# Optimization experiments

Hardware: AMD Instinct MI355X
Metric: run time of the kernel (lower is better)

Reference implementation:

```python
import jax, jax.numpy as jnp
import numpy as np

B, S, D, H = 2048, 200, 128, 4
H1, H2 = 64, 32
F = 4 * D
TIME_DECAY = 0.1


def setup_inputs() -> dict:
    key = jax.random.key(0)
    ks = jax.random.split(key, 10)
    query = jax.random.normal(ks[0], (B, D), dtype=jnp.float32)
    keys = jax.random.normal(ks[1], (B, S, D), dtype=jnp.float32)
    keys_mask = jax.random.randint(ks[2], (B, S), 0, 2).astype(bool)
    keys_mask = keys_mask.at[:, 0].set(True)  # avoid fully-masked rows
    sc = 0.02
    # per-head MLP params, stacked over heads
    W1 = sc * jax.random.normal(ks[3], (H, H1, F), dtype=jnp.float32)
    b1 = jnp.zeros((H, H1), dtype=jnp.float32)
    a1 = 0.25 * jnp.ones((H,), dtype=jnp.float32)  # PReLU (default single param)
    W2 = sc * jax.random.normal(ks[4], (H, H2, H1), dtype=jnp.float32)
    b2 = jnp.zeros((H, H2), dtype=jnp.float32)
    a2 = 0.25 * jnp.ones((H,), dtype=jnp.float32)
    W3 = sc * jax.random.normal(ks[5], (H, H2), dtype=jnp.float32)
    b3 = jnp.zeros((H,), dtype=jnp.float32)
    Wo = sc * jax.random.normal(ks[6], (D, D), dtype=jnp.float32)
    bo = jnp.zeros((D,), dtype=jnp.float32)
    return {"query": query, "keys": keys, "keys_mask": keys_mask,
            "W1": W1, "b1": b1, "a1": a1, "W2": W2, "b2": b2, "a2": a2,
            "W3": W3, "b3": b3, "Wo": Wo, "bo": bo}


def reference(query, keys, keys_mask, W1, b1, a1, W2, b2, a2, W3, b3, Wo, bo):
    b, s, d = keys.shape
    q = query[:, None, :]                                    # [B,1,D]
    x = jnp.concatenate(
        [keys, jnp.broadcast_to(q, (b, s, d)), keys * q, keys - q], axis=-1)  # [B,S,4D]
    pos = jnp.arange(s, dtype=keys.dtype)
    tw = jnp.exp(TIME_DECAY * (pos - s + 1))                 # [S]
    # all heads batched: [B,H,S,H1]
    h = jnp.einsum('bsf,hdf->bhsd', x, W1) + b1[None, :, None, :]
    h = jnp.where(h >= 0, h, a1[None, :, None, None] * h)    # PReLU
    h = jnp.einsum('bhsd,hed->bhse', h, W2) + b2[None, :, None, :]
    h = jnp.where(h >= 0, h, a2[None, :, None, None] * h)
    scores = jnp.einsum('bhse,he->bhs', h, W3) + b3[None, :, None]
    scores = scores * tw[None, None, :]
    scores = jnp.where(keys_mask[:, None, :], scores, -1e9)
    w = jax.nn.softmax(scores, axis=-1)                      # [B,H,S]
    out_h = jnp.einsum('bhs,bsd->bhd', w, keys)              # [B,H,D]
    combined = out_h.mean(axis=1)                            # [B,D]
    output = combined @ Wo.T + bo                            # [B,D]
    avg_weights = w.mean(axis=1)                             # [B,S]
    return output, avg_weights
```

## Files before the change

kernel.cpp:

```cpp
#include <hip/hip_runtime.h>
#include <hip/hip_bf16.h>
#include <stdint.h>

#define Bsz 2048
#define Ssz 200
#define Dsz 128

typedef __attribute__((ext_vector_type(8))) short short8;
typedef __attribute__((ext_vector_type(4))) short short4v;
typedef __attribute__((ext_vector_type(4))) float f32x4;
typedef unsigned short ushort_t;
typedef unsigned int uint_t;

#define KEYS_OFF   0
#define SCB_OFF    28672
#define C1S_OFF    30720
#define B2S_OFF    31744
#define W3S_OFF    32256
#define SMEM_A     32768

#if defined(__has_builtin)
#if __has_builtin(__builtin_amdgcn_mfma_f32_16x16x16bf16_1k)
#define HAVE_MFMA16 1
#endif
#endif

__device__ __forceinline__ f32x4 mfma16(short4v a, short4v b, f32x4 c) {
#ifdef HAVE_MFMA16
    return __builtin_amdgcn_mfma_f32_16x16x16bf16_1k(a, b, c, 0, 0, 0);
#else
    f32x4 d;
    asm volatile("v_mfma_f32_16x16x16_bf16 %0, %1, %2, %3"
                 : "=&v"(d) : "v"(a), "v"(b), "v"(c));
    return d;
#endif
}

__device__ __forceinline__ ushort_t cvtbf(float x) {
    __hip_bfloat16 h = __float2bfloat16(x);
    ushort_t u;
    __builtin_memcpy(&u, &h, 2);
    return u;
}
__device__ __forceinline__ float bflo(uint_t kv) {
    union { uint_t u; float f; } v; v.u = kv << 16; return v.f;
}
__device__ __forceinline__ float bfhi(uint_t kv) {
    union { uint_t u; float f; } v; v.u = kv & 0xFFFF0000u; return v.f;
}

__global__ void prep_kernel(const float* __restrict__ W1, const float* __restrict__ W2,
                            const float* __restrict__ Wo,
                            float* __restrict__ W1sum, float* __restrict__ W1c,
                            float* __restrict__ W1diffR, float* __restrict__ WoT,
                            ushort_t* __restrict__ W2bf) {
    int i = blockIdx.x * blockDim.x + threadIdx.x;
    if (i < 32768) {
        int n = i >> 7, j = i & 127;
        float a  = W1[n * 512 + j];
        float dd = W1[n * 512 + 384 + j];
        W1sum[i] = a + dd;
        W1c[i]   = W1[n * 512 + 256 + j];
        W1diffR[i] = W1[n * 512 + 128 + j] - dd;
    }
    if (i < 16384) {
        int j = i >> 7, d = i & 127;
        WoT[i] = Wo[d * 128 + j];
    }
    if (i < 8192) W2bf[i] = cvtbf(W2[i]);
}

__global__ void w1effc1_kernel(const float* __restrict__ query, const float* __restrict__ W1sum,
                               const float* __restrict__ W1c, const float* __restrict__ W1diffR,
                               const float* __restrict__ b1,
                               ushort_t* __restrict__ W1g2, float* __restrict__ c1out) {
    __shared__ float qs[128];
    int b = blockIdx.x, t = threadIdx.x;
    if (t < 128) qs[t] = query[b * 128 + t];
    __syncthreads();
    {
        float acc = b1[t];
        const float4* wr  = (const float4*)(W1diffR + t * 128);
        const float4* qv4 = (const float4*)qs;
        #pragma unroll 8
        for (int j4 = 0; j4 < 32; ++j4) {
            float4 wv = wr[j4];
            float4 qq = qv4[j4];
            acc += wv.x * qq.x + wv.y * qq.y + wv.z * qq.z + wv.w * qq.w;
        }
        c1out[b * 256 + t] = acc;
    }
    ushort_t* wout = W1g2 + ((size_t)b << 15);
    #pragma unroll 2
    for (int it = 0; it < 16; ++it) {
        int o  = t + 256 * it;
        int t4 = o >> 10, lk = (o >> 8) & 3, n = o & 255;
        int k0 = t4 * 32 + lk * 8;
        const float4* ps = (const float4*)(W1sum + n * 128 + k0);
        const float4* pc = (const float4*)(W1c + n * 128 + k0);
        const float4* pq = (const float4*)(qs + k0);
        float4 s0 = ps[0], s1 = ps[1];
        float4 c0 = pc[0], c1f = pc[1];
        float4 q0 = pq[0], q1 = pq[1];
        short8 ov;
        ov[0] = (short)cvtbf(s0.x + c0.x * q0.x);
        ov[1] = (short)cvtbf(s0.y + c0.y * q0.y);
        ov[2] = (short)cvtbf(s0.z + c0.z * q0.z);
        ov[3] = (short)cvtbf(s0.w + c0.w * q0.w);
        ov[4] = (short)cvtbf(s1.x + c1f.x * q1.x);
        ov[5] = (short)cvtbf(s1.y + c1f.y * q1.y);
        ov[6] = (short)cvtbf(s1.z + c1f.z * q1.z);
        ov[7] = (short)cvtbf(s1.w + c1f.w * q1.w);
        *(short8*)(wout + (size_t)o * 8) = ov;
    }
}

__global__ void c1_kernel(const float* __restrict__ query, const float* __restrict__ W1diffR,
                          const float* __restrict__ b1, float* __restrict__ c1out) {
    int b = blockIdx.x, n = threadIdx.x;
    float acc = b1[n];
    const float4* wr  = (const float4*)(W1diffR + n * 128);
    const float4* qv4 = (const float4*)(query + b * 128);
    #pragma unroll 8
    for (int j4 = 0; j4 < 32; ++j4) {
        float4 wv = wr[j4];
        float4 qq = qv4[j4];
        acc += wv.x * qq.x + wv.y * qq.y + wv.z * qq.z + wv.w * qq.w;
    }
    c1out[b * 256 + n] = acc;
}

__device__ __forceinline__ void stage_all(char* smem, const float* keys,
                                          const float* c1ws, const float* b2g,
                                          const float* w3g, int bb, int half, int tid) {
    const float* kb = keys + (size_t)bb * Ssz * Dsz;
    const int rbase = half * 112;
    #pragma unroll 2
    for (int it = 0; it < 14; ++it) {
        int id = tid + 256 * it;
        int row = id >> 5, c4 = id & 31;
        int grow = rbase + row;
        float4 kv = {0.f, 0.f, 0.f, 0.f};
        if (grow < Ssz) kv = *(const float4*)(kb + (size_t)grow * Dsz + c4 * 4);
        uint2 p;
        p.x = (uint_t)cvtbf(kv.x) | ((uint_t)cvtbf(kv.y) << 16);
        p.y = (uint_t)cvtbf(kv.z) | ((uint_t)cvtbf(kv.w) << 16);
        int off = KEYS_OFF + (((row << 8) + (c4 << 3)) ^ ((row & 7) << 4));
        *(uint2*)(smem + off) = p;
    }
    ((float*)(smem + C1S_OFF))[tid] = c1ws[bb * 256 + tid];
    if (tid < 128) ((float*)(smem + B2S_OFF))[tid] = b2g[tid];
    else if (tid < 256) ((float*)(smem + W3S_OFF))[tid - 128] = w3g[tid - 128];
}

__device__ __forceinline__ void scores_body(char* smem, const short8* bfr,
                                            const int* kmask,
                                            const float* a1, const float* a2,
                                            const float* b3, const ushort_t* W2bf,
                                            float* scores_ws,
                                            float* numws, float* mdws,
                                            int bb, int half, int w, int l, int l15, int lk) {
    const int rbase = half * 112;

    const float a1v = a1[w];
    const float a2v = a2[w];
    const float b3v = b3[w];
    short4v w2a[2][4];
    #pragma unroll
    for (int nt2 = 0; nt2 < 2; ++nt2)
        #pragma unroll
        for (int kt = 0; kt < 4; ++kt)
            w2a[nt2][kt] = *(const short4v*)(W2bf + w * 2048 + (nt2 * 16 + l15) * 64
                                             + kt * 16 + lk * 4);

    __syncthreads();

    const f32x4 fz = {0.f, 0.f, 0.f, 0.f};
    float* scb = (float*)(smem + SCB_OFF + w * 512);
    const float* c1s = (const float*)(smem + C1S_OFF);
    const float* b2s = (const float*)(smem + B2S_OFF);
    const float* w3s = (const float*)(smem + W3S_OFF);
    const int ntiles = 7 - half;

    #pragma unroll 1
    for (int mi = 0; mi < ntiles; ++mi) {
        f32x4 acc[4];
        #pragma unroll
        for (int kt = 0; kt < 4; ++kt) acc[kt] = fz;
        #pragma unroll
        for (int t = 0; t < 4; ++t) {
            int lrow = mi * 16 + l15;
            int off = KEYS_OFF + (((lrow << 8) + (t * 64 + lk * 16)) ^ ((lrow & 7) << 4));
            short8 kfr = *(const short8*)(smem + off);
            #pragma unroll
            for (int kt = 0; kt < 4; ++kt)
                acc[kt] = __builtin_amdgcn_mfma_f32_16x16x32_bf16(bfr[t * 4 + kt], kfr, acc[kt], 0, 0, 0);
        }
        short4v pa[4];
        #pragma unroll
        for (int kt = 0; kt < 4; ++kt) {
            f32x4 c1q = *(const f32x4*)(c1s + w * 64 + kt * 16 + lk * 4);
            #pragma unroll
            for (int r = 0; r < 4; ++r) {
                float v = acc[kt][r] + c1q[r];
                v = (v >= 0.f) ? v : a1v * v;
                pa[kt][r] = (short)cvtbf(v);
            }
        }
        f32x4 acc2[2];
        acc2[0] = fz; acc2[1] = fz;
        #pragma unroll
        for (int kt = 0; kt < 4; ++kt) {
            acc2[0] = mfma16(w2a[0][kt], pa[kt], acc2[0]);
            acc2[1] = mfma16(w2a[1][kt], pa[kt], acc2[1]);
        }
        float sum = 0.f;
        #pragma unroll
        for (int nt2 = 0; nt2 < 2; ++nt2) {
            f32x4 b2q = *(const f32x4*)(b2s + w * 32 + nt2 * 16 + lk * 4);
            f32x4 w3q = *(const f32x4*)(w3s + w * 32 + nt2 * 16 + lk * 4);
            #pragma unroll
            for (int r = 0; r < 4; ++r) {
                float v = acc2[nt2][r] + b2q[r];
                v = (v >= 0.f) ? v : a2v * v;
                sum += v * w3q[r];
            }
        }
        sum += __shfl_xor(sum, 16);
        sum += __shfl_xor(sum, 32);
        if (l < 16) {
            int sl = mi * 16 + l15;
            int sg = rbase + sl;
            if (sg < Ssz) {
                float tw = __expf(0.1f * (float)(sg - (Ssz - 1)));
                float sc = (sum + b3v) * tw;
                sc = kmask[bb * Ssz + sg] ? sc : -1.0e9f;
                scores_ws[bb * 800 + w * 200 + sg] = sc;
                scb[sl] = sc;
            } else {
                scb[sl] = -1.0e30f;
            }
        }
    }

    {
        int s0i = l, s1i = l + 64;
        bool v0 = (rbase + s0i < Ssz);
        bool v1 = (s1i < 112) && (rbase + s1i < Ssz);
        float x0 = v0 ? scb[s0i] : -1.0e30f;
        float x1 = v1 ? scb[s1i] : -1.0e30f;
        float m = fmaxf(x0, x1);
        #pragma unroll
        for (int mm = 1; mm < 64; mm <<= 1) m = fmaxf(m, __shfl_xor(m, mm));
        float e0 = v0 ? __expf(x0 - m) : 0.f;
        float e1 = v1 ? __expf(x1 - m) : 0.f;
        float dsum = e0 + e1;
        #pragma unroll
        for (int mm = 1; mm < 64; mm <<= 1) dsum += __shfl_xor(dsum, mm);
        scb[s0i] = e0;
        if (s1i < 112) scb[s1i] = e1;
        int g = l >> 5, dq = l & 31;
        float n0 = 0.f, n1 = 0.f, n2 = 0.f, n3 = 0.f;
        const int sb = g * 56;
        #pragma unroll 4
        for (int si = 0; si < 56; ++si) {
            int s = sb + si;
            float wv = scb[s];
            uint2 kv = *(const uint2*)(smem + KEYS_OFF + (((s << 8) + 8 * dq) ^ ((s & 7) << 4)));
            n0 += wv * bflo(kv.x);
            n1 += wv * bfhi(kv.x);
            n2 += wv * bflo(kv.y);
            n3 += wv * bfhi(kv.y);
        }
        n0 += __shfl_xor(n0, 32);
        n1 += __shfl_xor(n1, 32);
        n2 += __shfl_xor(n2, 32);
        n3 += __shfl_xor(n3, 32);
        if (l < 32) {
            size_t base = ((size_t)(bb * 4 + w) * 2 + half) * 128;
            float4 o; o.x = n0; o.y = n1; o.z = n2; o.w = n3;
            *(float4*)(numws + base + 4 * dq) = o;
        }
        if (l == 0) {
            mdws[((bb * 4 + w) * 2 + half) * 2]     = m;
            mdws[((bb * 4 + w) * 2 + half) * 2 + 1] = dsum;
        }
    }
}

__launch_bounds__(256, 3)
__global__ void scores_w1g(const float* __restrict__ keys, const int* __restrict__ kmask,
                           const float* __restrict__ a1, const float* __restrict__ b2,
                           const float* __restrict__ a2, const float* __restrict__ W3,
                           const float* __restrict__ b3,
                           const ushort_t* __restrict__ W2bf, const float* __restrict__ c1ws,
                           const ushort_t* __restrict__ W1g2, float* __restrict__ scores_ws,
                           float* __restrict__ numws, float* __restrict__ mdws) {
    extern __shared__ char smem[];
    const int tid  = threadIdx.x;
    const int bb   = blockIdx.x >> 1;
    const int half = blockIdx.x & 1;
    const int w   = tid >> 6;
    const int l   = tid & 63;
    const int l15 = l & 15;
    const int lk  = l >> 4;

    stage_all(smem, keys, c1ws, b2, W3, bb, half, tid);
    __builtin_amdgcn_sched_barrier(0);

    short8 bfr[16];
    const ushort_t* w1p = W1g2 + ((size_t)bb << 15);
    #pragma unroll
    for (int t = 0; t < 4; ++t)
        #pragma unroll
        for (int nt = 0; nt < 4; ++nt)
            bfr[t * 4 + nt] = *(const short8*)(w1p +
                (size_t)((t * 4 + lk) * 256 + w * 64 + nt * 16 + l15) * 8);

    scores_body(smem, bfr, kmask, a1, a2, b3, W2bf, scores_ws,
                numws, mdws, bb, half, w, l, l15, lk);
}

__launch_bounds__(256, 2)
__global__ void scores_fold(const float* __restrict__ query, const float* __restrict__ keys,
                            const int* __restrict__ kmask,
                            const float* __restrict__ a1, const float* __restrict__ b2,
                            const float* __restrict__ a2, const float* __restrict__ W3,
                            const float* __restrict__ b3,
                            const float* __restrict__ W1sum, const float* __restrict__ W1c,
                            const ushort_t* __restrict__ W2bf, const float* __restrict__ c1ws,
                            float* __restrict__ scores_ws,
                            float* __restrict__ numws, float* __restrict__ mdws) {
    extern __shared__ char smem[];
    const int tid  = threadIdx.x;
    const int bb   = blockIdx.x >> 1;
    const int half = blockIdx.x & 1;
    const int w   = tid >> 6;
    const int l   = tid & 63;
    const int l15 = l & 15;
    const int lk  = l >> 4;

    stage_all(smem, keys, c1ws, b2, W3, bb, half, tid);
    __builtin_amdgcn_sched_barrier(0);

    short8 bfr[16];
    #pragma unroll
    for (int t = 0; t < 4; ++t) {
        const int k0 = t * 32 + lk * 8;
        const float4* pq = (const float4*)(query + bb * 128 + k0);
        float4 q0 = pq[0], q1 = pq[1];
        #pragma unroll
        for (int nt = 0; nt < 4; ++nt) {
            int n = w * 64 + nt * 16 + l15;
            const float4* ps = (const float4*)(W1sum + n * 128 + k0);
            const float4* pc = (const float4*)(W1c + n * 128 + k0);
            float4 s0 = ps[0], s1 = ps[1];
            float4 c0 = pc[0], c1f = pc[1];
            short8 ov;
            ov[0] = (short)cvtbf(s0.x + c0.x * q0.x);
            ov[1] = (short)cvtbf(s0.y + c0.y * q0.y);
            ov[2] = (short)cvtbf(s0.z + c0.z * q0.z);
            ov[3] = (short)cvtbf(s0.w + c0.w * q0.w);
            ov[4] = (short)cvtbf(s1.x + c1f.x * q1.x);
            ov[5] = (short)cvtbf(s1.y + c1f.y * q1.y);
            ov[6] = (short)cvtbf(s1.z + c1f.z * q1.z);
            ov[7] = (short)cvtbf(s1.w + c1f.w * q1.w);
            bfr[t * 4 + nt] = ov;
        }
    }

    scores_body(smem, bfr, kmask, a1, a2, b3, W2bf, scores_ws,
                numws, mdws, bb, half, w, l, l15, lk);
}

__launch_bounds__(256, 4)
__global__ void finish_comb(const float* __restrict__ scores_ws, const float* __restrict__ numws,
                            const float* __restrict__ mdws, const float* __restrict__ WoT,
                            const float* __restrict__ bo, float* __restrict__ out) {
    __shared__ float scw[4][224];
    __shared__ float comb[128];
    __shared__ float po2[2][128];

    const int tid = threadIdx.x;
    const int bb  = blockIdx.x;
    const int w   = tid >> 6;
    const int l   = tid & 63;

    {
        float xv[4], wv[4];
        float mx = -3.0e38f;
        #pragma unroll
        for (int i = 0; i < 4; ++i) {
            int s = l + 64 * i;
            xv[i] = (s < Ssz) ? scores_ws[bb * 800 + w * 200 + s] : -1.0e30f;
            mx = fmaxf(mx, xv[i]);
        }
        #pragma unroll
        for (int m = 1; m < 64; m <<= 1) mx = fmaxf(mx, __shfl_xor(mx, m));
        float sm = 0.f;
        #pragma unroll
        for (int i = 0; i < 4; ++i) {
            int s = l + 64 * i;
            wv[i] = (s < Ssz) ? __expf(xv[i] - mx) : 0.f;
            sm += wv[i];
        }
        #pragma unroll
        for (int m = 1; m < 64; m <<= 1) sm += __shfl_xor(sm, m);
        float inv = 1.0f / sm;
        #pragma unroll
        for (int i = 0; i < 4; ++i) {
            int s = l + 64 * i;
            if (s < Ssz) scw[w][s] = wv[i] * inv;
        }
    }
    __syncthreads();

    if (tid < Ssz) {
        float aw = 0.25f * (scw[0][tid] + scw[1][tid] + scw[2][tid] + scw[3][tid]);
        out[Bsz * Dsz + bb * Ssz + tid] = aw;
    }

    if (tid < 128) {
        float c = 0.f;
        #pragma unroll
        for (int h = 0; h < 4; ++h) {
            int mb = ((bb * 4 + h) * 2) * 2;
            float m0 = mdws[mb], d0 = mdws[mb + 1];
            float m1 = mdws[mb + 2], d1 = mdws[mb + 3];
            float m = fmaxf(m0, m1);
            float a0 = __expf(m0 - m), a1 = __expf(m1 - m);
            float den = d0 * a0 + d1 * a1;
            size_t nb = (size_t)((bb * 4 + h) * 2) * 128;
            c += (numws[nb + tid] * a0 + numws[nb + 128 + tid] * a1) / den;
        }
        comb[tid] = 0.25f * c;
    }
    __syncthreads();

    {
        int d = tid & 127, part = tid >> 7;
        float o = 0.f;
        const float* wp = WoT + (size_t)part * 64 * 128 + d;
        #pragma unroll 8
        for (int j = 0; j < 64; ++j) o += comb[part * 64 + j] * wp[j * 128];
        po2[part][d] = o;
    }
    __syncthreads();
    if (tid < 128) out[bb * Dsz + tid] = bo[tid] + po2[0][tid] + po2[1][tid];
}

extern "C" void kernel_launch(void* const* d_in, const int* in_sizes, int n_in,
                              void* d_out, int out_size, void* d_ws, size_t ws_size,
                              hipStream_t stream) {
    const float* query = (const float*)d_in[0];
    const float* keys  = (const float*)d_in[1];
    const int*   kmask = (const int*)d_in[2];
    const float* W1    = (const float*)d_in[3];
    const float* b1    = (const float*)d_in[4];
    const float* a1    = (const float*)d_in[5];
    const float* W2    = (const float*)d_in[6];
    const float* b2    = (const float*)d_in[7];
    const float* a2    = (const float*)d_in[8];
    const float* W3    = (const float*)d_in[9];
    const float* b3    = (const float*)d_in[10];
    const float* Wo    = (const float*)d_in[11];
    const float* bo    = (const float*)d_in[12];
    float* out = (float*)d_out;

    char* ws = (char*)d_ws;
    float*    W1sum   = (float*)(ws);
    float*    W1c     = (float*)(ws + 131072);
    float*    W1diffR = (float*)(ws + 262144);
    float*    WoT     = (float*)(ws + 393216);
    ushort_t* W2bf    = (ushort_t*)(ws + 458752);
    float*    c1ws    = (float*)(ws + 475136);
    float*    scores  = (float*)(ws + 2572288);
    float*    numws   = (float*)(ws + 9125888);
    float*    mdws    = (float*)(ws + 17514496);
    ushort_t* W1g2    = (ushort_t*)(ws + 17645568);

    const bool useW1G = ws_size >= (size_t)17645568 + (size_t)Bsz * 32768 * 2;

    prep_kernel<<<128, 256, 0, stream>>>(W1, W2, Wo, W1sum, W1c, W1diffR, WoT, W2bf);

    if (useW1G) {
        hipFuncSetAttribute(reinterpret_cast<const void*>(scores_w1g),
                            hipFuncAttributeMaxDynamicSharedMemorySize, SMEM_A);
        w1effc1_kernel<<<Bsz, 256, 0, stream>>>(query, W1sum, W1c, W1diffR, b1, W1g2, c1ws);
        scores_w1g<<<Bsz * 2, 256, SMEM_A, stream>>>(keys, kmask, a1, b2, a2, W3, b3,
                                                     W2bf, c1ws, W1g2, scores, numws, mdws);
    } else {
        hipFuncSetAttribute(reinterpret_cast<const void*>(scores_fold),
                            hipFuncAttributeMaxDynamicSharedMemorySize, SMEM_A);
        c1_kernel<<<Bsz, 256, 0, stream>>>(query, W1diffR, b1, c1ws);
        scores_fold<<<Bsz * 2, 256, SMEM_A, stream>>>(query, keys, kmask, a1, b2, a2, W3, b3,
                                                      W1sum, W1c, W2bf, c1ws, scores,
                                                      numws, mdws);
    }
    finish_comb<<<Bsz, 256, 0, stream>>>(scores, numws, mdws, WoT, bo, out);
}
```

Baseline: 223.3 us.

## Drop materialized per-batch W1 path and always fold query into W1 in-kernel

Removes the path that wrote a per-batch bf16 effective W1 matrix (128 MB) to workspace and read it back in the scores kernel. Now the fold-in variant, which builds the W1 fragments from W1sum/W1c and the query inside the scores kernel, always runs. It also raises the launch bound from 2 to 3 blocks per CU. This trades the large global write/read traffic for extra per-block ALU work and repeated reads of the shared W1sum/W1c tables, which should hit in cache.

Result: slower. 229.5 us (+2.8%).

```diff
diff --git a/kernel.cpp b/kernel.cpp
--- a/kernel.cpp
+++ b/kernel.cpp
@@ -68,51 +68,6 @@
         WoT[i] = Wo[d * 128 + j];
     }
     if (i < 8192) W2bf[i] = cvtbf(W2[i]);
-}
-
-__global__ void w1effc1_kernel(const float* __restrict__ query, const float* __restrict__ W1sum,
-                               const float* __restrict__ W1c, const float* __restrict__ W1diffR,
-                               const float* __restrict__ b1,
-                               ushort_t* __restrict__ W1g2, float* __restrict__ c1out) {
-    __shared__ float qs[128];
-    int b = blockIdx.x, t = threadIdx.x;
-    if (t < 128) qs[t] = query[b * 128 + t];
-    __syncthreads();
-    {
-        float acc = b1[t];
-        const float4* wr  = (const float4*)(W1diffR + t * 128);
-        const float4* qv4 = (const float4*)qs;
-        #pragma unroll 8
-        for (int j4 = 0; j4 < 32; ++j4) {
-            float4 wv = wr[j4];
-            float4 qq = qv4[j4];
-            acc += wv.x * qq.x + wv.y * qq.y + wv.z * qq.z + wv.w * qq.w;
-        }
-        c1out[b * 256 + t] = acc;
-    }
-    ushort_t* wout = W1g2 + ((size_t)b << 15);
-    #pragma unroll 2
-    for (int it = 0; it < 16; ++it) {
-        int o  = t + 256 * it;
-        int t4 = o >> 10, lk = (o >> 8) & 3, n = o & 255;
-        int k0 = t4 * 32 + lk * 8;
-        const float4* ps = (const float4*)(W1sum + n * 128 + k0);
-        const float4* pc = (const float4*)(W1c + n * 128 + k0);
-        const float4* pq = (const float4*)(qs + k0);
-        float4 s0 = ps[0], s1 = ps[1];
-        float4 c0 = pc[0], c1f = pc[1];
-        float4 q0 = pq[0], q1 = pq[1];
-        short8 ov;
-        ov[0] = (short)cvtbf(s0.x + c0.x * q0.x);
-        ov[1] = (short)cvtbf(s0.y + c0.y * q0.y);
-        ov[2] = (short)cvtbf(s0.z + c0.z * q0.z);
-        ov[3] = (short)cvtbf(s0.w + c0.w * q0.w);
-        ov[4] = (short)cvtbf(s1.x + c1f.x * q1.x);
-        ov[5] = (short)cvtbf(s1.y + c1f.y * q1.y);
-        ov[6] = (short)cvtbf(s1.z + c1f.z * q1.z);
-        ov[7] = (short)cvtbf(s1.w + c1f.w * q1.w);
-        *(short8*)(wout + (size_t)o * 8) = ov;
-    }
 }
 
 __global__ void c1_kernel(const float* __restrict__ query, const float* __restrict__ W1diffR,
@@ -153,149 +108,16 @@
     else if (tid < 256) ((float*)(smem + W3S_OFF))[tid - 128] = w3g[tid - 128];
 }
 
-__device__ __forceinline__ void scores_body(char* smem, const short8* bfr,
-                                            const int* kmask,
-                                            const float* a1, const float* a2,
-                                            const float* b3, const ushort_t* W2bf,
-                                            float* scores_ws,
-                                            float* numws, float* mdws,
-                                            int bb, int half, int w, int l, int l15, int lk) {
-    const int rbase = half * 112;
-
-    const float a1v = a1[w];
-    const float a2v = a2[w];
-    const float b3v = b3[w];
-    short4v w2a[2][4];
-    #pragma unroll
-    for (int nt2 = 0; nt2 < 2; ++nt2)
-        #pragma unroll
-        for (int kt = 0; kt < 4; ++kt)
-            w2a[nt2][kt] = *(const short4v*)(W2bf + w * 2048 + (nt2 * 16 + l15) * 64
-                                             + kt * 16 + lk * 4);
-
-    __syncthreads();
-
-    const f32x4 fz = {0.f, 0.f, 0.f, 0.f};
-    float* scb = (float*)(smem + SCB_OFF + w * 512);
-    const float* c1s = (const float*)(smem + C1S_OFF);
-    const float* b2s = (const float*)(smem + B2S_OFF);
-    const float* w3s = (const float*)(smem + W3S_OFF);
-    const int ntiles = 7 - half;
-
-    #pragma unroll 1
-    for (int mi = 0; mi < ntiles; ++mi) {
-        f32x4 acc[4];
-        #pragma unroll
-        for (int kt = 0; kt < 4; ++kt) acc[kt] = fz;
-        #pragma unroll
-        for (int t = 0; t < 4; ++t) {
-            int lrow = mi * 16 + l15;
-            int off = KEYS_OFF + (((lrow << 8) + (t * 64 + lk * 16)) ^ ((lrow & 7) << 4));
-            short8 kfr = *(const short8*)(smem + off);
-            #pragma unroll
-            for (int kt = 0; kt < 4; ++kt)
-                acc[kt] = __builtin_amdgcn_mfma_f32_16x16x32_bf16(bfr[t * 4 + kt], kfr, acc[kt], 0, 0, 0);
-        }
-        short4v pa[4];
-        #pragma unroll
-        for (int kt = 0; kt < 4; ++kt) {
-            f32x4 c1q = *(const f32x4*)(c1s + w * 64 + kt * 16 + lk * 4);
-            #pragma unroll
-            for (int r = 0; r < 4; ++r) {
-                float v = acc[kt][r] + c1q[r];
-                v = (v >= 0.f) ? v : a1v * v;
-                pa[kt][r] = (short)cvtbf(v);
-            }
-        }
-        f32x4 acc2[2];
-        acc2[0] = fz; acc2[1] = fz;
-        #pragma unroll
-        for (int kt = 0; kt < 4; ++kt) {
-            acc2[0] = mfma16(w2a[0][kt], pa[kt], acc2[0]);
-            acc2[1] = mfma16(w2a[1][kt], pa[kt], acc2[1]);
-        }
-        float sum = 0.f;
-        #pragma unroll
-        for (int nt2 = 0; nt2 < 2; ++nt2) {
-            f32x4 b2q = *(const f32x4*)(b2s + w * 32 + nt2 * 16 + lk * 4);
-            f32x4 w3q = *(const f32x4*)(w3s + w * 32 + nt2 * 16 + lk * 4);
-            #pragma unroll
-            for (int r = 0; r < 4; ++r) {
-                float v = acc2[nt2][r] + b2q[r];
-                v = (v >= 0.f) ? v : a2v * v;
-                sum += v * w3q[r];
-            }
-        }
-        sum += __shfl_xor(sum, 16);
-        sum += __shfl_xor(sum, 32);
-        if (l < 16) {
-            int sl = mi * 16 + l15;
-            int sg = rbase + sl;
-            if (sg < Ssz) {
-                float tw = __expf(0.1f * (float)(sg - (Ssz - 1)));
-                float sc = (sum + b3v) * tw;
-                sc = kmask[bb * Ssz + sg] ? sc : -1.0e9f;
-                scores_ws[bb * 800 + w * 200 + sg] = sc;
-                scb[sl] = sc;
-            } else {
-                scb[sl] = -1.0e30f;
-            }
-        }
-    }
-
-    {
-        int s0i = l, s1i = l + 64;
-        bool v0 = (rbase + s0i < Ssz);
-        bool v1 = (s1i < 112) && (rbase + s1i < Ssz);
-        float x0 = v0 ? scb[s0i] : -1.0e30f;
-        float x1 = v1 ? scb[s1i] : -1.0e30f;
-        float m = fmaxf(x0, x1);
-        #pragma unroll
-        for (int mm = 1; mm < 64; mm <<= 1) m = fmaxf(m, __shfl_xor(m, mm));
-        float e0 = v0 ? __expf(x0 - m) : 0.f;
-        float e1 = v1 ? __expf(x1 - m) : 0.f;
-        float dsum = e0 + e1;
-        #pragma unroll
-        for (int mm = 1; mm < 64; mm <<= 1) dsum += __shfl_xor(dsum, mm);
-        scb[s0i] = e0;
-        if (s1i < 112) scb[s1i] = e1;
-        int g = l >> 5, dq = l & 31;
-        float n0 = 0.f, n1 = 0.f, n2 = 0.f, n3 = 0.f;
-        const int sb = g * 56;
-        #pragma unroll 4
-        for (int si = 0; si < 56; ++si) {
-            int s = sb + si;
-            float wv = scb[s];
-            uint2 kv = *(const uint2*)(smem + KEYS_OFF + (((s << 8) + 8 * dq) ^ ((s & 7) << 4)));
-            n0 += wv * bflo(kv.x);
-            n1 += wv * bfhi(kv.x);
-            n2 += wv * bflo(kv.y);
-            n3 += wv * bfhi(kv.y);
-        }
-        n0 += __shfl_xor(n0, 32);
-        n1 += __shfl_xor(n1, 32);
-        n2 += __shfl_xor(n2, 32);
-        n3 += __shfl_xor(n3, 32);
-        if (l < 32) {
-            size_t base = ((size_t)(bb * 4 + w) * 2 + half) * 128;
-            float4 o; o.x = n0; o.y = n1; o.z = n2; o.w = n3;
-            *(float4*)(numws + base + 4 * dq) = o;
-        }
-        if (l == 0) {
-            mdws[((bb * 4 + w) * 2 + half) * 2]     = m;
-            mdws[((bb * 4 + w) * 2 + half) * 2 + 1] = dsum;
-        }
-    }
-}
-
 __launch_bounds__(256, 3)
-__global__ void scores_w1g(const float* __restrict__ keys, const int* __restrict__ kmask,
-                           const float* __restrict__ a1, const float* __restrict__ b2,
-                           const float* __restrict__ a2, const float* __restrict__ W3,
-                           const float* __restrict__ b3,
-                           const ushort_t* __restrict__ W2bf, const float* __restrict__ c1ws,
-                           const ushort_t* __restrict__ W1g2, float* __restrict__ scores_ws,
-                           float* __restrict__ numws, float* __restrict__ mdws) {
+__global__ void scores_kernel(const float* __restrict__ query, const float* __restrict__ keys,
+                              const int* __restrict__ kmask,
+                              const float* __restrict__ a1, const float* __restrict__ b2,
+                              const float* __restrict__ a2, const float* __restrict__ W3,
+                              const float* __restrict__ b3,
+                              const float* __restrict__ W1sum, const float* __restrict__ W1c,
+                              const ushort_t* __restrict__ W2bf, const float* __restrict__ c1ws,
+                              float* __restrict__ scores_ws,
+                              float* __restrict__ numws, float* __restrict__ mdws) {
     extern __shared__ char smem[];
     const int tid  = threadIdx.x;
     const int bb   = blockIdx.x >> 1;
@@ -304,41 +126,7 @@
     const int l   = tid & 63;
     const int l15 = l & 15;
     const int lk  = l >> 4;
-
-    stage_all(smem, keys, c1ws, b2, W3, bb, half, tid);
-    __builtin_amdgcn_sched_barrier(0);
-
-    short8 bfr[16];
-    const ushort_t* w1p = W1g2 + ((size_t)bb << 15);
-    #pragma unroll
-    for (int t = 0; t < 4; ++t)
-        #pragma unroll
-        for (int nt = 0; nt < 4; ++nt)
-            bfr[t * 4 + nt] = *(const short8*)(w1p +
-                (size_t)((t * 4 + lk) * 256 + w * 64 + nt * 16 + l15) * 8);
-
-    scores_body(smem, bfr, kmask, a1, a2, b3, W2bf, scores_ws,
-                numws, mdws, bb, half, w, l, l15, lk);
-}
-
-__launch_bounds__(256, 2)
-__global__ void scores_fold(const float* __restrict__ query, const float* __restrict__ keys,
-                            const int* __restrict__ kmask,
-                            const float* __restrict__ a1, const float* __restrict__ b2,
-                            const float* __restrict__ a2, const float* __restrict__ W3,
-                            const float* __restrict__ b3,
-                            const float* __restrict__ W1sum, const float* __restrict__ W1c,
-                            const ushort_t* __restrict__ W2bf, const float* __restrict__ c1ws,
-                            float* __restrict__ scores_ws,
-                            float* __restrict__ numws, float* __restrict__ mdws) {
-    extern __shared__ char smem[];
-    const int tid  = threadIdx.x;
-    const int bb   = blockIdx.x >> 1;
-    const int half = blockIdx.x & 1;
-    const int w   = tid >> 6;
-    const int l   = tid & 63;
-    const int l15 = l & 15;
-    const int lk  = l >> 4;
+    const int rbase = half * 112;
 
     stage_all(smem, keys, c1ws, b2, W3, bb, half, tid);
     __builtin_amdgcn_sched_barrier(0);
@@ -369,8 +157,130 @@
         }
     }
 
-    scores_body(smem, bfr, kmask, a1, a2, b3, W2bf, scores_ws,
-                numws, mdws, bb, half, w, l, l15, lk);
+    const float a1v = a1[w];
+    const float a2v = a2[w];
+    const float b3v = b3[w];
+    short4v w2a[2][4];
+    #pragma unroll
+    for (int nt2 = 0; nt2 < 2; ++nt2)
+        #pragma unroll
+        for (int kt = 0; kt < 4; ++kt)
+            w2a[nt2][kt] = *(const short4v*)(W2bf + w * 2048 + (nt2 * 16 + l15) * 64
+                                             + kt * 16 + lk * 4);
+
+    __syncthreads();
+
+    const f32x4 fz = {0.f, 0.f, 0.f, 0.f};
+    float* scb = (float*)(smem + SCB_OFF + w * 512);
+    const float* c1s = (const float*)(smem + C1S_OFF);
+    const float* b2s = (const float*)(smem + B2S_OFF);
+    const float* w3s = (const float*)(smem + W3S_OFF);
+    const int ntiles = 7 - half;
+
+    #pragma unroll 1
+    for (int mi = 0; mi < ntiles; ++mi) {
+        f32x4 acc[4];
+        #pragma unroll
+        for (int kt = 0; kt < 4; ++kt) acc[kt] = fz;
+        #pragma unroll
+        for (int t = 0; t < 4; ++t) {
+            int lrow = mi * 16 + l15;
+            int off = KEYS_OFF + (((lrow << 8) + (t * 64 + lk * 16)) ^ ((lrow & 7) << 4));
+            short8 kfr = *(const short8*)(smem + off);
+            #pragma unroll
+            for (int kt = 0; kt < 4; ++kt)
+                acc[kt] = __builtin_amdgcn_mfma_f32_16x16x32_bf16(bfr[t * 4 + kt], kfr, acc[kt], 0, 0, 0);
+        }
+        short4v pa[4];
+        #pragma unroll
+        for (int kt = 0; kt < 4; ++kt) {
+            f32x4 c1q = *(const f32x4*)(c1s + w * 64 + kt * 16 + lk * 4);
+            #pragma unroll
+            for (int r = 0; r < 4; ++r) {
+                float v = acc[kt][r] + c1q[r];
+                v = (v >= 0.f) ? v : a1v * v;
+                pa[kt][r] = (short)cvtbf(v);
+            }
+        }
+        f32x4 acc2[2];
+        acc2[0] = fz; acc2[1] = fz;
+        #pragma unroll
+        for (int kt = 0; kt < 4; ++kt) {
+            acc2[0] = mfma16(w2a[0][kt], pa[kt], acc2[0]);
+            acc2[1] = mfma16(w2a[1][kt], pa[kt], acc2[1]);
+        }
+        float sum = 0.f;
+        #pragma unroll
+        for (int nt2 = 0; nt2 < 2; ++nt2) {
+            f32x4 b2q = *(const f32x4*)(b2s + w * 32 + nt2 * 16 + lk * 4);
+            f32x4 w3q = *(const f32x4*)(w3s + w * 32 + nt2 * 16 + lk * 4);
+            #pragma unroll
+            for (int r = 0; r < 4; ++r) {
+                float v = acc2[nt2][r] + b2q[r];
+                v = (v >= 0.f) ? v : a2v * v;
+                sum += v * w3q[r];
+            }
+        }
+        sum += __shfl_xor(sum, 16);
+        sum += __shfl_xor(sum, 32);
+        if (l < 16) {
+            int sl = mi * 16 + l15;
+            int sg = rbase + sl;
+            if (sg < Ssz) {
+                float tw = __expf(0.1f * (float)(sg - (Ssz - 1)));
+                float sc = (sum + b3v) * tw;
+                sc = kmask[bb * Ssz + sg] ? sc : -1.0e9f;
+                scores_ws[bb * 800 + w * 200 + sg] = sc;
+                scb[sl] = sc;
+            } else {
+                scb[sl] = -1.0e30f;
+            }
+        }
+    }
+
+    {
+        int s0i = l, s1i = l + 64;
+        bool v0 = (rbase + s0i < Ssz);
+        bool v1 = (s1i < 112) && (rbase + s1i < Ssz);
+        float x0 = v0 ? scb[s0i] : -1.0e30f;
+        float x1 = v1 ? scb[s1i] : -1.0e30f;
+        float m = fmaxf(x0, x1);
+        #pragma unroll
+        for (int mm = 1; mm < 64; mm <<= 1) m = fmaxf(m, __shfl_xor(m, mm));
+        float e0 = v0 ? __expf(x0 - m) : 0.f;
+        float e1 = v1 ? __expf(x1 - m) : 0.f;
+        float dsum = e0 + e1;
+        #pragma unroll
+        for (int mm = 1; mm < 64; mm <<= 1) dsum += __shfl_xor(dsum, mm);
+        scb[s0i] = e0;
+        if (s1i < 112) scb[s1i] = e1;
+        int g = l >> 5, dq = l & 31;
+        float n0 = 0.f, n1 = 0.f, n2 = 0.f, n3 = 0.f;
+        const int sb = g * 56;
+        #pragma unroll 4
+        for (int si = 0; si < 56; ++si) {
+            int s = sb + si;
+            float wv = scb[s];
+            uint2 kv = *(const uint2*)(smem + KEYS_OFF + (((s << 8) + 8 * dq) ^ ((s & 7) << 4)));
+            n0 += wv * bflo(kv.x);
+            n1 += wv * bfhi(kv.x);
+            n2 += wv * bflo(kv.y);
+            n3 += wv * bfhi(kv.y);
+        }
+        n0 += __shfl_xor(n0, 32);
+        n1 += __shfl_xor(n1, 32);
+        n2 += __shfl_xor(n2, 32);
+        n3 += __shfl_xor(n3, 32);
+        if (l < 32) {
+            size_t base = ((size_t)(bb * 4 + w) * 2 + half) * 128;
+            float4 o; o.x = n0; o.y = n1; o.z = n2; o.w = n3;
+            *(float4*)(numws + base + 4 * dq) = o;
+        }
+        if (l == 0) {
+            mdws[((bb * 4 + w) * 2 + half) * 2]     = m;
+            mdws[((bb * 4 + w) * 2 + half) * 2 + 1] = dsum;
+        }
+    }
 }
 
 __launch_bounds__(256, 4)
@@ -477,25 +387,14 @@
     float*    scores  = (float*)(ws + 2572288);
     float*    numws   = (float*)(ws + 9125888);
     float*    mdws    = (float*)(ws + 17514496);
-    ushort_t* W1g2    = (ushort_t*)(ws + 17645568);
-
-    const bool useW1G = ws_size >= (size_t)17645568 + (size_t)Bsz * 32768 * 2;
+
+    hipFuncSetAttribute(reinterpret_cast<const void*>(scores_kernel),
+                        hipFuncAttributeMaxDynamicSharedMemorySize, SMEM_A);
 
     prep_kernel<<<128, 256, 0, stream>>>(W1, W2, Wo, W1sum, W1c, W1diffR, WoT, W2bf);
-
-    if (useW1G) {
-        hipFuncSetAttribute(reinterpret_cast<const void*>(scores_w1g),
-                            hipFuncAttributeMaxDynamicSharedMemorySize, SMEM_A);
-        w1effc1_kernel<<<Bsz, 256, 0, stream>>>(query, W1sum, W1c, W1diffR, b1, W1g2, c1ws);
-        scores_w1g<<<Bsz * 2, 256, SMEM_A, stream>>>(keys, kmask, a1, b2, a2, W3, b3,
-                                                     W2bf, c1ws, W1g2, scores, numws, mdws);
-    } else {
-        hipFuncSetAttribute(reinterpret_cast<const void*>(scores_fold),
-                            hipFuncAttributeMaxDynamicSharedMemorySize, SMEM_A);
-        c1_kernel<<<Bsz, 256, 0, stream>>>(query, W1diffR, b1, c1ws);
-        scores_fold<<<Bsz * 2, 256, SMEM_A, stream>>>(query, keys, kmask, a1, b2, a2, W3, b3,
-                                                      W1sum, W1c, W2bf, c1ws, scores,
-                                                      numws, mdws);
-    }
+    c1_kernel<<<Bsz, 256, 0, stream>>>(query, W1diffR, b1, c1ws);
+    scores_kernel<<<Bsz * 2, 256, SMEM_A, stream>>>(query, keys, kmask, a1, b2, a2, W3, b3,
+                                                    W1sum, W1c, W2bf, c1ws, scores,
+                                                    numws, mdws);
     finish_comb<<<Bsz, 256, 0, stream>>>(scores, numws, mdws, WoT, bo, out);
 }
```
